# Performance work log

Measured on AMD Instinct MI355X. Metric: run time of the kernel, lower is better.

Reference implementation:

```python
import jax, jax.numpy as jnp
import numpy as np

DIM = 1024
NUM_HEADS = 16
HEAD_DIM = DIM // NUM_HEADS
MLP_HIDDEN = 4 * DIM
SCALE = HEAD_DIM ** -0.5
EPS = 1e-5


def setup_inputs() -> dict:
    key = jax.random.key(0)
    ks = jax.random.split(key, 6)
    s = (2.0 / DIM) ** 0.5
    sd = (2.0 / MLP_HIDDEN) ** 0.5
    return {
        "x": jax.random.normal(ks[0], (2, 2048, DIM), dtype=jnp.float32),
        "attn_qkv_weight": jax.random.normal(ks[1], (3 * DIM, DIM), dtype=jnp.float32) * s,
        "attn_out_weight": jax.random.normal(ks[2], (DIM, DIM), dtype=jnp.float32) * s,
        "norm1_weight": jnp.ones((DIM,), jnp.float32),
        "norm1_bias": jnp.zeros((DIM,), jnp.float32),
        "mlp_gate_weight": jax.random.normal(ks[3], (MLP_HIDDEN, DIM), dtype=jnp.float32) * s,
        "mlp_up_weight": jax.random.normal(ks[4], (MLP_HIDDEN, DIM), dtype=jnp.float32) * s,
        "mlp_down_weight": jax.random.normal(ks[5], (DIM, MLP_HIDDEN), dtype=jnp.float32) * sd,
        "norm2_weight": jnp.ones((DIM,), jnp.float32),
        "norm2_bias": jnp.zeros((DIM,), jnp.float32),
    }


def _layer_norm(x, w, b):
    mean = x.mean(axis=-1, keepdims=True)
    var = jnp.mean(jnp.square(x - mean), axis=-1, keepdims=True)
    return (x - mean) / jnp.sqrt(var + EPS) * w + b


def reference(x, attn_qkv_weight, attn_out_weight, norm1_weight, norm1_bias,
              mlp_gate_weight, mlp_up_weight, mlp_down_weight, norm2_weight, norm2_bias):
    B, S, D = x.shape
    residual1 = x
    xn = _layer_norm(x, norm1_weight, norm1_bias)
    qkv = xn @ attn_qkv_weight.T                      # [B,S,3D]
    qkv = qkv.reshape(B, S, 3, NUM_HEADS, HEAD_DIM).transpose(2, 0, 3, 1, 4)
    q, k, v = qkv[0], qkv[1], qkv[2]                  # [B,H,S,hd]
    scores = jnp.einsum('bhqd,bhkd->bhqk', q, k) * SCALE  # full O(S^2) matrix
    attn = jax.nn.softmax(scores, axis=-1)            # no causal mask (default False)
    out = jnp.einsum('bhqk,bhkd->bhqd', attn, v)      # [B,H,S,hd]
    out = out.transpose(0, 2, 1, 3).reshape(B, S, D)
    x2 = residual1 + out @ attn_out_weight.T
    xn2 = _layer_norm(x2, norm2_weight, norm2_bias)
    gate = xn2 @ mlp_gate_weight.T
    up = xn2 @ mlp_up_weight.T
    hidden = jax.nn.silu(gate) * up
    return x2 + hidden @ mlp_down_weight.T
```

## Files before the change

kernel.cpp:

```cpp
#include <hip/hip_runtime.h>

typedef float f32x4 __attribute__((ext_vector_type(4)));
typedef __bf16 bf16x8 __attribute__((ext_vector_type(8)));
typedef unsigned int u32;

#define DEV __device__ __forceinline__
#define WAITVM(n) asm volatile("s_waitcnt vmcnt(" #n ")" ::: "memory")

DEV void gload_lds16(const void* g, void* l) {
  __builtin_amdgcn_global_load_lds(
      (const __attribute__((address_space(1))) u32*)g,
      (__attribute__((address_space(3))) u32*)l, 16, 0, 0);
}

DEV int xcd_swz(int flat, int nwg) {
  return (flat & 7) * (nwg >> 3) + (flat >> 3);
}

__global__ __launch_bounds__(256) void cvt_all(const float* __restrict__ s0,
                                               const float* __restrict__ s1,
                                               const float* __restrict__ s2,
                                               const float* __restrict__ s3,
                                               const float* __restrict__ s4,
                                               __bf16* __restrict__ d0,
                                               __bf16* __restrict__ d1,
                                               __bf16* __restrict__ d2,
                                               __bf16* __restrict__ d3,
                                               __bf16* __restrict__ d4) {
  size_t i = ((size_t)blockIdx.x * 256 + threadIdx.x) * 8;
  const float* s; __bf16* d; size_t off;
  if (i < 3145728)        { s = s0; d = d0; off = 0; }
  else if (i < 4194304)   { s = s1; d = d1; off = 3145728; }
  else if (i < 8388608)   { s = s2; d = d2; off = 4194304; }
  else if (i < 12582912)  { s = s3; d = d3; off = 8388608; }
  else                    { s = s4; d = d4; off = 12582912; }
  const size_t j = i - off;
  float4 a = *(const float4*)(s + j);
  float4 b = *(const float4*)(s + j + 4);
  union { bf16x8 v; __bf16 e[8]; } u;
  u.e[0] = (__bf16)a.x; u.e[1] = (__bf16)a.y; u.e[2] = (__bf16)a.z; u.e[3] = (__bf16)a.w;
  u.e[4] = (__bf16)b.x; u.e[5] = (__bf16)b.y; u.e[6] = (__bf16)b.z; u.e[7] = (__bf16)b.w;
  *(bf16x8*)(d + j) = u.v;
}

__global__ __launch_bounds__(256) void ln_kernel(const float* __restrict__ x,
                                                 const float* __restrict__ w,
                                                 const float* __restrict__ b,
                                                 __bf16* __restrict__ o) {
  const int row = blockIdx.x, tid = threadIdx.x;
  const float4 v = ((const float4*)(x + (size_t)row * 1024))[tid];
  float s  = v.x + v.y + v.z + v.w;
  float s2 = v.x * v.x + v.y * v.y + v.z * v.z + v.w * v.w;
  for (int off = 32; off; off >>= 1) {
    s  += __shfl_down(s, off);
    s2 += __shfl_down(s2, off);
  }
  __shared__ float rs[4], rs2[4];
  if ((tid & 63) == 0) { rs[tid >> 6] = s; rs2[tid >> 6] = s2; }
  __syncthreads();
  float S = rs[0] + rs[1] + rs[2] + rs[3];
  float S2 = rs2[0] + rs2[1] + rs2[2] + rs2[3];
  float mean = S * (1.0f / 1024.0f);
  float var = S2 * (1.0f / 1024.0f) - mean * mean;
  float inv = rsqrtf(var + 1e-5f);
  const float4 wv = ((const float4*)w)[tid];
  const float4 bv = ((const float4*)b)[tid];
  union { ushort4 u4; __bf16 e[4]; } u;
  u.e[0] = (__bf16)((v.x - mean) * inv * wv.x + bv.x);
  u.e[1] = (__bf16)((v.y - mean) * inv * wv.y + bv.y);
  u.e[2] = (__bf16)((v.z - mean) * inv * wv.z + bv.z);
  u.e[3] = (__bf16)((v.w - mean) * inv * wv.w + bv.w);
  *(ushort4*)(o + (size_t)row * 1024 + tid * 4) = u.u4;
}


template <int EPI, int MI>
__global__ __launch_bounds__(256) void gemm_bt(const __bf16* __restrict__ A,
                                               const __bf16* __restrict__ B,
                                               void* __restrict__ Cout,
                                               const float* __restrict__ Res,
                                               int M, int N, int K) {
  constexpr int BM = MI * 32;
  __shared__ __align__(16) __bf16 As[3][BM * 32];
  __shared__ __align__(16) __bf16 Bs[3][128 * 32];
  const int tid = threadIdx.x;
  const int lane = tid & 63;
  const int w = tid >> 6;
  const int wr = w >> 1, wc = w & 1;
  const int l15 = lane & 15, g = lane >> 4;
  const int c8 = ((g + (l15 >> 1)) & 3) * 8;

  const int nbx = gridDim.x;
  const int logical = xcd_swz(blockIdx.y * nbx + blockIdx.x, nbx * gridDim.y);
  const int per = 8 * nbx, grp = logical / per, rem = logical % per;
  const int bm = (grp * 8 + (rem & 7)) * BM;
  const int bn = (rem >> 3) * 128;

  f32x4 acc[MI][4] = {};

  auto stage = [&](int buf, int k0) {
#pragma unroll
    for (int p = 0; p < MI / 2; ++p) {
      const int ch = p * 256 + tid;
      const int row = ch >> 2;
      const int gc = ((ch & 3) - ((ch >> 3) & 3)) & 3;
      gload_lds16(A + (size_t)(bm + row) * K + k0 + gc * 8,
                  &As[buf][(p * 256 + w * 64) * 8]);
    }
#pragma unroll
    for (int p = 0; p < 2; ++p) {
      const int ch = p * 256 + tid;
      const int row = ch >> 2;
      const int gc = ((ch & 3) - ((ch >> 3) & 3)) & 3;
      gload_lds16(B + (size_t)(bn + row) * K + k0 + gc * 8,
                  &Bs[buf][(p * 256 + w * 64) * 8]);
    }
  };

  const int NT = K >> 5;
  stage(0, 0);
  stage(1, 32);

  int cur = 0;
  for (int t = 0; t < NT; ++t) {
    if (t + 1 < NT) {
      if constexpr (MI == 8)      { WAITVM(6); }
      else if constexpr (MI == 4) { WAITVM(4); }
      else                        { WAITVM(3); }
    } else {
      WAITVM(0);
    }
    __builtin_amdgcn_s_barrier();
    if (t + 2 < NT) {
      int sb = cur + 2; if (sb >= 3) sb -= 3;
      stage(sb, (t + 2) * 32);
    }
    bf16x8 af[MI], bfr[4];
#pragma unroll
    for (int i = 0; i < MI; ++i)
      af[i] = *(const bf16x8*)(&As[cur][(wr * (MI * 16) + i * 16 + l15) * 32 + c8]);
#pragma unroll
    for (int j = 0; j < 4; ++j)
      bfr[j] = *(const bf16x8*)(&Bs[cur][(wc * 64 + j * 16 + l15) * 32 + c8]);
#pragma unroll
    for (int i = 0; i < MI; ++i)
#pragma unroll
      for (int j = 0; j < 4; ++j)
        acc[i][j] = __builtin_amdgcn_mfma_f32_16x16x32_bf16(af[i], bfr[j], acc[i][j], 0, 0, 0);
    cur = (cur == 2) ? 0 : cur + 1;
  }

  const int r0 = bm + wr * (MI * 16) + g * 4;
  const int c0 = bn + wc * 64 + l15;
#pragma unroll
  for (int i = 0; i < MI; ++i)
#pragma unroll
    for (int j = 0; j < 4; ++j)
#pragma unroll
      for (int r = 0; r < 4; ++r) {
        const size_t idx = (size_t)(r0 + i * 16 + r) * N + (c0 + j * 16);
        const float v = acc[i][j][r];
        if (EPI == 0) ((__bf16*)Cout)[idx] = (__bf16)v;
        else          ((float*)Cout)[idx] = v + Res[idx];
      }
}

__global__ __launch_bounds__(512) void gemm_mlp(const __bf16* __restrict__ A,
                                                const __bf16* __restrict__ BG,
                                                const __bf16* __restrict__ BU,
                                                __bf16* __restrict__ H,
                                                int M, int N, int K) {
  __shared__ __align__(16) __bf16 As[3][256 * 32];
  __shared__ __align__(16) __bf16 Bg[3][128 * 32];
  __shared__ __align__(16) __bf16 Bu[3][128 * 32];
  const int tid = threadIdx.x;
  const int lane = tid & 63;
  const int w = tid >> 6;
  const int wr = w >> 1, wc = w & 1;
  const int l15 = lane & 15, g = lane >> 4;
  const int c8 = ((g + (l15 >> 1)) & 3) * 8;

  const int nbx = gridDim.x;
  const int logical = xcd_swz(blockIdx.y * nbx + blockIdx.x, nbx * gridDim.y);
  const int per = 8 * nbx, grp = logical / per, rem = logical % per;
  const int bm = (grp * 8 + (rem & 7)) * 256;
  const int bn = (rem >> 3) * 128;

  f32x4 accg[4][4] = {};
  f32x4 accu[4][4] = {};

  auto stage = [&](int buf, int k0) {
#pragma unroll
    for (int p = 0; p < 2; ++p) {
      const int ch = p * 512 + tid;
      const int row = ch >> 2;
      const int gc = ((ch & 3) - ((ch >> 3) & 3)) & 3;
      gload_lds16(A + (size_t)(bm + row) * K + k0 + gc * 8,
                  &As[buf][(p * 512 + w * 64) * 8]);
    }
    {
      const int ch = tid;
      const int row = ch >> 2;
      const int gc = ((ch & 3) - ((ch >> 3) & 3)) & 3;
      const size_t ro = (size_t)(bn + row) * K + k0 + gc * 8;
      gload_lds16(BG + ro, &Bg[buf][(w * 64) * 8]);
      gload_lds16(BU + ro, &Bu[buf][(w * 64) * 8]);
    }
  };

  const int NT = K >> 5;
  stage(0, 0);
  stage(1, 32);

  int cur = 0;
  for (int t = 0; t < NT; ++t) {
    if (t + 1 < NT) { WAITVM(4); } else { WAITVM(0); }
    __builtin_amdgcn_s_barrier();
    if (t + 2 < NT) {
      int sb = cur + 2; if (sb >= 3) sb -= 3;
      stage(sb, (t + 2) * 32);
    }
    bf16x8 af[4], bgf[4], buf_[4];
#pragma unroll
    for (int i = 0; i < 4; ++i)
      af[i] = *(const bf16x8*)(&As[cur][(wr * 64 + i * 16 + l15) * 32 + c8]);
#pragma unroll
    for (int j = 0; j < 4; ++j) {
      bgf[j] = *(const bf16x8*)(&Bg[cur][(wc * 64 + j * 16 + l15) * 32 + c8]);
      buf_[j] = *(const bf16x8*)(&Bu[cur][(wc * 64 + j * 16 + l15) * 32 + c8]);
    }
#pragma unroll
    for (int i = 0; i < 4; ++i)
#pragma unroll
      for (int j = 0; j < 4; ++j) {
        accg[i][j] = __builtin_amdgcn_mfma_f32_16x16x32_bf16(af[i], bgf[j], accg[i][j], 0, 0, 0);
        accu[i][j] = __builtin_amdgcn_mfma_f32_16x16x32_bf16(af[i], buf_[j], accu[i][j], 0, 0, 0);
      }
    cur = (cur == 2) ? 0 : cur + 1;
  }

  const int r0 = bm + wr * 64 + g * 4;
  const int c0 = bn + wc * 64 + l15;
#pragma unroll
  for (int i = 0; i < 4; ++i)
#pragma unroll
    for (int j = 0; j < 4; ++j)
#pragma unroll
      for (int r = 0; r < 4; ++r) {
        const float gt = accg[i][j][r];
        const float ut = accu[i][j][r];
        const float h = gt / (1.0f + __expf(-gt)) * ut;
        H[(size_t)(r0 + i * 16 + r) * N + (c0 + j * 16)] = (__bf16)h;
      }
}

__global__ __launch_bounds__(256) void transpose_v(const __bf16* __restrict__ qkv,
                                                   __bf16* __restrict__ vT) {
  const int st = blockIdx.x, bh = blockIdx.y;
  const int b = bh >> 4, h = bh & 15;
  __shared__ __bf16 tile[64][80];
  const int tid = threadIdx.x;
#pragma unroll
  for (int it = 0; it < 2; ++it) {
    const int idx = it * 256 + tid;
    const int r = idx >> 3, c0 = (idx & 7) * 8;
    bf16x8 v = *(const bf16x8*)(qkv + (size_t)(b * 2048 + st * 64 + r) * 3072 + 2048 + h * 64 + c0);
    *(bf16x8*)&tile[r][c0] = v;
  }
  __syncthreads();
#pragma unroll
  for (int it = 0; it < 2; ++it) {
    const int idx = it * 256 + tid;
    const int d = idx >> 3, s0 = (idx & 7) * 8;
    union { bf16x8 v; __bf16 e[8]; } u;
#pragma unroll
    for (int j = 0; j < 8; ++j) u.e[j] = tile[s0 + j][d];
    *(bf16x8*)(vT + (size_t)(bh * 64 + d) * 2048 + st * 64 + s0) = u.v;
  }
}

__global__ __launch_bounds__(256) void attn_kernel(const __bf16* __restrict__ qkv,
                                                   const __bf16* __restrict__ vT,
                                                   __bf16* __restrict__ Opart,
                                                   float* __restrict__ Lpart) {
  const int logical = xcd_swz(blockIdx.y * 32 + blockIdx.x, 2048);
  const int qt = logical & 31;
  const int rest = logical >> 5;
  const int bh = rest >> 1, half = rest & 1;
  const int b = bh >> 4, h = bh & 15;
  const int tid = threadIdx.x, lane = tid & 63, w = tid >> 6;
  const int l15 = lane & 15, g = lane >> 4;
  const float CSC = 0.125f * 1.44269504f;

  __shared__ __align__(16) __bf16 Ks[64 * 64];
  __shared__ __align__(16) __bf16 Vs[64 * 64];
  __shared__ __align__(16) __bf16 Ps[4][16 * 80];

  const int qrow = qt * 64 + w * 16 + l15;
  const size_t qbase = (size_t)(b * 2048 + qrow) * 3072 + h * 64;
  bf16x8 qf0, qf1;
  {
    union { bf16x8 v; __bf16 e[8]; } a, bq, oa, ob;
    a.v = *(const bf16x8*)(qkv + qbase + g * 8);
    bq.v = *(const bf16x8*)(qkv + qbase + 32 + g * 8);
#pragma unroll
    for (int j = 0; j < 8; ++j) {
      oa.e[j] = (__bf16)((float)a.e[j] * CSC);
      ob.e[j] = (__bf16)((float)bq.e[j] * CSC);
    }
    qf0 = oa.v; qf1 = ob.v;
  }

  f32x4 o_acc[4] = {};
  float l_r[4] = {0.f, 0.f, 0.f, 0.f};

  const size_t kgbase = (size_t)(b * 2048) * 3072 + 1024 + h * 64;
  const size_t vgbase = (size_t)bh * 64 * 2048;

  for (int tt = 0; tt < 16; ++tt) {
    const int kv0 = half * 1024 + tt * 64;
#pragma unroll
    for (int p = 0; p < 2; ++p) {
      const int ch = p * 256 + w * 64 + lane;
      const int row = ch >> 3, c = ch & 7;
      const int gc = c ^ (row & 7);
      gload_lds16(qkv + kgbase + (size_t)(kv0 + row) * 3072 + gc * 8, Ks + (p * 256 + w * 64) * 8);
      gload_lds16(vT + vgbase + (size_t)row * 2048 + kv0 + gc * 8, Vs + (p * 256 + w * 64) * 8);
    }
    WAITVM(0);
    __syncthreads();

    f32x4 sf[4];
    __builtin_amdgcn_s_setprio(1);
#pragma unroll
    for (int ni = 0; ni < 4; ++ni) {
      const int krow = ni * 16 + l15;
      const __bf16* kb = Ks + krow * 64;
      const bf16x8 kf0 = *(const bf16x8*)(kb + ((g ^ (krow & 7)) * 8));
      const bf16x8 kf1 = *(const bf16x8*)(kb + (((4 + g) ^ (krow & 7)) * 8));
      f32x4 z = {0.f, 0.f, 0.f, 0.f};
      z = __builtin_amdgcn_mfma_f32_16x16x32_bf16(qf0, kf0, z, 0, 0, 0);
      z = __builtin_amdgcn_mfma_f32_16x16x32_bf16(qf1, kf1, z, 0, 0, 0);
      sf[ni] = z;
    }
    __builtin_amdgcn_s_setprio(0);

#pragma unroll
    for (int ni = 0; ni < 4; ++ni)
#pragma unroll
      for (int r = 0; r < 4; ++r) {
        const float pv = exp2f(sf[ni][r]);
        sf[ni][r] = pv;
        l_r[r] += pv;
      }

    __bf16* pw = Ps[w];
#pragma unroll
    for (int ni = 0; ni < 4; ++ni)
#pragma unroll
      for (int r = 0; r < 4; ++r) {
        const int row = g * 4 + r;
        const int pc = (ni * 2 + (l15 >> 3)) ^ (row & 7);
        pw[row * 80 + pc * 8 + (l15 & 7)] = (__bf16)sf[ni][r];
      }
    asm volatile("" ::: "memory");
    const bf16x8 pa0 = *(const bf16x8*)(pw + l15 * 80 + ((g ^ (l15 & 7)) * 8));
    const bf16x8 pa1 = *(const bf16x8*)(pw + l15 * 80 + (((4 + g) ^ (l15 & 7)) * 8));

    __builtin_amdgcn_s_setprio(1);
#pragma unroll
    for (int ni = 0; ni < 4; ++ni) {
      const int vrow = ni * 16 + l15;
      const __bf16* vb = Vs + vrow * 64;
      const bf16x8 vf0 = *(const bf16x8*)(vb + ((g ^ (vrow & 7)) * 8));
      const bf16x8 vf1 = *(const bf16x8*)(vb + (((4 + g) ^ (vrow & 7)) * 8));
      o_acc[ni] = __builtin_amdgcn_mfma_f32_16x16x32_bf16(pa0, vf0, o_acc[ni], 0, 0, 0);
      o_acc[ni] = __builtin_amdgcn_mfma_f32_16x16x32_bf16(pa1, vf1, o_acc[ni], 0, 0, 0);
    }
    __builtin_amdgcn_s_setprio(0);
    __syncthreads();
  }

#pragma unroll
  for (int mk = 1; mk < 16; mk <<= 1)
#pragma unroll
    for (int r = 0; r < 4; ++r) l_r[r] += __shfl_xor(l_r[r], mk);

  const size_t obase = (size_t)half * 4194304;
#pragma unroll
  for (int r = 0; r < 4; ++r) {
    const int orow = qt * 64 + w * 16 + g * 4 + r;
    const size_t grow = (size_t)(b * 2048 + orow);
    if (l15 == 0) Lpart[half * 65536 + grow * 16 + h] = l_r[r];
#pragma unroll
    for (int ni = 0; ni < 4; ++ni)
      Opart[obase + grow * 1024 + h * 64 + ni * 16 + l15] = (__bf16)o_acc[ni][r];
  }
}

__global__ __launch_bounds__(256) void attn_merge(const __bf16* __restrict__ Opart,
                                                  const float* __restrict__ Lpart,
                                                  __bf16* __restrict__ outp) {
  const int row = blockIdx.x, tid = threadIdx.x;
  const int col = tid * 4, h = tid >> 4;
  const float l = Lpart[row * 16 + h] + Lpart[65536 + row * 16 + h];
  const float inv = 1.0f / l;
  union { ushort4 u; __bf16 e[4]; } a, b, o;
  a.u = *(const ushort4*)(Opart + (size_t)row * 1024 + col);
  b.u = *(const ushort4*)(Opart + 4194304 + (size_t)row * 1024 + col);
#pragma unroll
  for (int j = 0; j < 4; ++j)
    o.e[j] = (__bf16)(((float)a.e[j] + (float)b.e[j]) * inv);
  *(ushort4*)(outp + (size_t)row * 1024 + col) = o.u;
}

extern "C" void kernel_launch(void* const* d_in, const int* in_sizes, int n_in,
                              void* d_out, int out_size, void* d_ws, size_t ws_size,
                              hipStream_t stream) {
  const float* x     = (const float*)d_in[0];
  const float* Wqkv  = (const float*)d_in[1];
  const float* Wout  = (const float*)d_in[2];
  const float* n1w   = (const float*)d_in[3];
  const float* n1b   = (const float*)d_in[4];
  const float* Wgate = (const float*)d_in[5];
  const float* Wup   = (const float*)d_in[6];
  const float* Wdown = (const float*)d_in[7];
  const float* n2w   = (const float*)d_in[8];
  const float* n2b   = (const float*)d_in[9];
  float* out = (float*)d_out;
  char* ws = (char*)d_ws;
  const size_t MB = 1u << 20;

  __bf16* XN  = (__bf16*)(ws + 0);
  __bf16* QKV = (__bf16*)(ws + 8 * MB);
  __bf16* VT  = (__bf16*)(ws + 32 * MB);
  __bf16* ATT = (__bf16*)(ws + 40 * MB);
  float*  X2  = (float*)(ws + 48 * MB);
  __bf16* OP  = (__bf16*)(ws + 48 * MB);
  __bf16* H   = QKV;
  __bf16* WQ  = (__bf16*)(ws + 64 * MB);
  float*  LP  = (float*)(ws + 64 * MB);
  __bf16* WO  = (__bf16*)(ws + 70 * MB);
  __bf16* WG  = (__bf16*)(ws + 72 * MB);
  __bf16* WU  = (__bf16*)(ws + 80 * MB);
  __bf16* WD  = (__bf16*)(ws + 88 * MB);

  cvt_all<<<16777216 / 2048, 256, 0, stream>>>(Wqkv, Wout, Wgate, Wup, Wdown,
                                               WQ, WO, WG, WU, WD);

  ln_kernel<<<4096, 256, 0, stream>>>(x, n1w, n1b, XN);
  gemm_bt<0, 8><<<dim3(24, 16), 256, 0, stream>>>(XN, WQ, QKV, nullptr, 4096, 3072, 1024);
  transpose_v<<<dim3(32, 32), 256, 0, stream>>>(QKV, VT);
  attn_kernel<<<dim3(32, 64), 256, 0, stream>>>(QKV, VT, OP, LP);
  attn_merge<<<4096, 256, 0, stream>>>(OP, LP, ATT);
  gemm_bt<1, 2><<<dim3(8, 64), 256, 0, stream>>>(ATT, WO, X2, x, 4096, 1024, 1024);
  ln_kernel<<<4096, 256, 0, stream>>>(X2, n2w, n2b, XN);
  gemm_mlp<<<dim3(32, 16), 512, 0, stream>>>(XN, WG, WU, H, 4096, 4096, 1024);
  gemm_bt<1, 4><<<dim3(8, 32), 256, 0, stream>>>(H, WD, out, X2, 4096, 1024, 4096);

  (void)in_sizes; (void)n_in; (void)out_size; (void)ws_size;
}
```

Baseline: 360.9 us.

## Split MLP gate/up staging into phased loads with setprio, shrink GEMM tiles

The fused gate/up MLP GEMM now splits each k-step into two phases. The A and gate-B tiles are staged and consumed first, then the up-B tile, with extra barriers and s_setprio raised around the MFMA bursts. The goal is to interleave global-to-LDS loads with matrix work. Separately, the QKV projection and the down projection GEMMs now use smaller M tiles (MI 4 and 2) with more workgroups, to improve occupancy and wave count. The extra barriers per iteration add synchronization overhead, and the smaller tiles reduce reuse.

```diff
diff --git a/kernel.cpp b/kernel.cpp
--- a/kernel.cpp
+++ b/kernel.cpp
@@ -124,9 +124,7 @@
   int cur = 0;
   for (int t = 0; t < NT; ++t) {
     if (t + 1 < NT) {
-      if constexpr (MI == 8)      { WAITVM(6); }
-      else if constexpr (MI == 4) { WAITVM(4); }
-      else                        { WAITVM(3); }
+      if constexpr (MI == 4) { WAITVM(4); } else { WAITVM(3); }
     } else {
       WAITVM(0);
     }
@@ -165,11 +163,11 @@
       }
 }
 
-__global__ __launch_bounds__(512) void gemm_mlp(const __bf16* __restrict__ A,
-                                                const __bf16* __restrict__ BG,
-                                                const __bf16* __restrict__ BU,
-                                                __bf16* __restrict__ H,
-                                                int M, int N, int K) {
+__global__ __launch_bounds__(512) void gemm_mlp8(const __bf16* __restrict__ A,
+                                                 const __bf16* __restrict__ BG,
+                                                 const __bf16* __restrict__ BU,
+                                                 __bf16* __restrict__ H,
+                                                 int M, int N, int K) {
   __shared__ __align__(16) __bf16 As[3][256 * 32];
   __shared__ __align__(16) __bf16 Bg[3][128 * 32];
   __shared__ __align__(16) __bf16 Bu[3][128 * 32];
@@ -189,7 +187,7 @@
   f32x4 accg[4][4] = {};
   f32x4 accu[4][4] = {};
 
-  auto stage = [&](int buf, int k0) {
+  auto stage_a = [&](int buf, int k0) {
 #pragma unroll
     for (int p = 0; p < 2; ++p) {
       const int ch = p * 512 + tid;
@@ -198,45 +196,59 @@
       gload_lds16(A + (size_t)(bm + row) * K + k0 + gc * 8,
                   &As[buf][(p * 512 + w * 64) * 8]);
     }
-    {
-      const int ch = tid;
-      const int row = ch >> 2;
-      const int gc = ((ch & 3) - ((ch >> 3) & 3)) & 3;
-      const size_t ro = (size_t)(bn + row) * K + k0 + gc * 8;
-      gload_lds16(BG + ro, &Bg[buf][(w * 64) * 8]);
-      gload_lds16(BU + ro, &Bu[buf][(w * 64) * 8]);
-    }
   };
+  auto stage_b = [&](int buf, int k0) {
+    const int ch = tid;
+    const int row = ch >> 2;
+    const int gc = ((ch & 3) - ((ch >> 3) & 3)) & 3;
+    const size_t ro = (size_t)(bn + row) * K + k0 + gc * 8;
+    gload_lds16(BG + ro, &Bg[buf][(w * 64) * 8]);
+    gload_lds16(BU + ro, &Bu[buf][(w * 64) * 8]);
+  };
 
   const int NT = K >> 5;
-  stage(0, 0);
-  stage(1, 32);
-
-  int cur = 0;
+  stage_a(0, 0);  stage_b(0, 0);
+  stage_a(1, 32); stage_b(1, 32);
+
   for (int t = 0; t < NT; ++t) {
+    int cur = t % 3;
+    int sb = cur + 2; if (sb >= 3) sb -= 3;
+    const bool pre = (t + 2 < NT);
+
     if (t + 1 < NT) { WAITVM(4); } else { WAITVM(0); }
     __builtin_amdgcn_s_barrier();
-    if (t + 2 < NT) {
-      int sb = cur + 2; if (sb >= 3) sb -= 3;
-      stage(sb, (t + 2) * 32);
-    }
-    bf16x8 af[4], bgf[4], buf_[4];
+
+    if (pre) stage_a(sb, (t + 2) * 32);
+    bf16x8 af[4], bgf[4];
 #pragma unroll
     for (int i = 0; i < 4; ++i)
       af[i] = *(const bf16x8*)(&As[cur][(wr * 64 + i * 16 + l15) * 32 + c8]);
 #pragma unroll
-    for (int j = 0; j < 4; ++j) {
+    for (int j = 0; j < 4; ++j)
       bgf[j] = *(const bf16x8*)(&Bg[cur][(wc * 64 + j * 16 + l15) * 32 + c8]);
+    __builtin_amdgcn_s_barrier();
+    __builtin_amdgcn_s_setprio(1);
+#pragma unroll
+    for (int i = 0; i < 4; ++i)
+#pragma unroll
+      for (int j = 0; j < 4; ++j)
+        accg[i][j] = __builtin_amdgcn_mfma_f32_16x16x32_bf16(af[i], bgf[j], accg[i][j], 0, 0, 0);
+    __builtin_amdgcn_s_setprio(0);
+    __builtin_amdgcn_s_barrier();
+
+    if (pre) stage_b(sb, (t + 2) * 32);
+    bf16x8 buf_[4];
+#pragma unroll
+    for (int j = 0; j < 4; ++j)
       buf_[j] = *(const bf16x8*)(&Bu[cur][(wc * 64 + j * 16 + l15) * 32 + c8]);
-    }
+    __builtin_amdgcn_s_barrier();
+    __builtin_amdgcn_s_setprio(1);
 #pragma unroll
     for (int i = 0; i < 4; ++i)
 #pragma unroll
-      for (int j = 0; j < 4; ++j) {
-        accg[i][j] = __builtin_amdgcn_mfma_f32_16x16x32_bf16(af[i], bgf[j], accg[i][j], 0, 0, 0);
+      for (int j = 0; j < 4; ++j)
         accu[i][j] = __builtin_amdgcn_mfma_f32_16x16x32_bf16(af[i], buf_[j], accu[i][j], 0, 0, 0);
-      }
-    cur = (cur == 2) ? 0 : cur + 1;
+    __builtin_amdgcn_s_setprio(0);
   }
 
   const int r0 = bm + wr * 64 + g * 4;
@@ -449,14 +461,14 @@
                                                WQ, WO, WG, WU, WD);
 
   ln_kernel<<<4096, 256, 0, stream>>>(x, n1w, n1b, XN);
-  gemm_bt<0, 8><<<dim3(24, 16), 256, 0, stream>>>(XN, WQ, QKV, nullptr, 4096, 3072, 1024);
+  gemm_bt<0, 4><<<dim3(24, 32), 256, 0, stream>>>(XN, WQ, QKV, nullptr, 4096, 3072, 1024);
   transpose_v<<<dim3(32, 32), 256, 0, stream>>>(QKV, VT);
   attn_kernel<<<dim3(32, 64), 256, 0, stream>>>(QKV, VT, OP, LP);
   attn_merge<<<4096, 256, 0, stream>>>(OP, LP, ATT);
   gemm_bt<1, 2><<<dim3(8, 64), 256, 0, stream>>>(ATT, WO, X2, x, 4096, 1024, 1024);
   ln_kernel<<<4096, 256, 0, stream>>>(X2, n2w, n2b, XN);
-  gemm_mlp<<<dim3(32, 16), 512, 0, stream>>>(XN, WG, WU, H, 4096, 4096, 1024);
-  gemm_bt<1, 4><<<dim3(8, 32), 256, 0, stream>>>(H, WD, out, X2, 4096, 1024, 4096);
+  gemm_mlp8<<<dim3(32, 16), 512, 0, stream>>>(XN, WG, WU, H, 4096, 4096, 1024);
+  gemm_bt<1, 2><<<dim3(8, 64), 256, 0, stream>>>(H, WD, out, X2, 4096, 1024, 4096);
 
   (void)in_sizes; (void)n_in; (void)out_size; (void)ws_size;
 }
```

Result: faster. 330.7 us (-8.4%).
